# Optimization experiments

Measured on AMD Instinct MI355X. Metric: run time of the kernel, lower is better.

Reference implementation:

```python
import jax, jax.numpy as jnp
import numpy as np
import math

IN_CH = 512
OUT_CH = 512
KSIZE = 3
W_DIM = 512
CONV_SCALE = 1.0 / math.sqrt(IN_CH * KSIZE * KSIZE)
MOD_SCALE = 1.0 / math.sqrt(W_DIM)


def setup_inputs() -> dict:
    key = jax.random.key(0)
    k1, k2, k3, k4 = jax.random.split(key, 4)
    B, H, W = 16, 64, 64
    return {
        "input": jax.random.normal(k1, (B, IN_CH, H, W), dtype=jnp.float32),
        "style": jax.random.normal(k2, (B, W_DIM), dtype=jnp.float32),
        "weight": jax.random.normal(k3, (1, OUT_CH, IN_CH, KSIZE, KSIZE), dtype=jnp.float32),
        "mod_weight": jax.random.normal(k4, (IN_CH, W_DIM), dtype=jnp.float32),
        "mod_bias": jnp.ones((IN_CH,), dtype=jnp.float32),
    }


def reference(input, style, weight, mod_weight, mod_bias):
    B, Cin, H, Wd = input.shape
    # EqualLinear modulation: style -> per-sample, per-input-channel scale
    s = style @ (mod_weight * MOD_SCALE).T + mod_bias  # [B, Cin]
    s = s[:, None, :, None, None]                      # [B,1,Cin,1,1]
    w = CONV_SCALE * weight * s                        # [B,Cout,Cin,k,k]
    demod = jax.lax.rsqrt(jnp.sum(w * w, axis=(2, 3, 4)) + 1e-8)  # [B,Cout]
    w = w * demod[:, :, None, None, None]
    # Grouped conv with groups=batch, same as torch F.conv2d
    w = w.reshape(B * OUT_CH, Cin, KSIZE, KSIZE)
    x = input.reshape(1, B * Cin, H, Wd)
    pad = KSIZE // 2
    out = jax.lax.conv_general_dilated(
        x, w,
        window_strides=(1, 1),
        padding=[(pad, pad), (pad, pad)],
        dimension_numbers=("NCHW", "OIHW", "NCHW"),
        feature_group_count=B,
    )
    return out.reshape(B, OUT_CH, out.shape[2], out.shape[3])
```

## Files before the change

### kernel.cpp

```cpp
#include <hip/hip_runtime.h>
#include <hip/hip_bf16.h>


constexpr float CONV_SCALE = 0.014731391274719738f;
constexpr float MOD_SCALE  = 0.04419417382415922f;

typedef short  bf16x8 __attribute__((ext_vector_type(8)));
typedef float  f32x4  __attribute__((ext_vector_type(4)));

__device__ __forceinline__ unsigned short f2bf(float f) {
  unsigned u = __float_as_uint(f);
  u += 0x7fffu + ((u >> 16) & 1u);
  return (unsigned short)(u >> 16);
}

__device__ __forceinline__ void async16(const void* g, void* l) {
  __builtin_amdgcn_global_load_lds((const __attribute__((address_space(1))) unsigned int*)g,
                                   (__attribute__((address_space(3))) unsigned int*)l,
                                   16, 0, 0);
}

__global__ void k_style(const float* __restrict__ style, const float* __restrict__ mw,
                        const float* __restrict__ mb, float* __restrict__ s) {
  int t = blockIdx.x * 256 + threadIdx.x;
  int b = t & 15, i = t >> 4;
  const float4* st = (const float4*)(style + b * 512);
  const float4* wr = (const float4*)(mw + i * 512);
  float acc = 0.f;
#pragma unroll 8
  for (int j = 0; j < 128; ++j) {
    float4 a = st[j], w4 = wr[j];
    acc += a.x * w4.x + a.y * w4.y + a.z * w4.z + a.w * w4.w;
  }
  s[b * 512 + i] = acc * MOD_SCALE + mb[i];
}

__global__ void k_prepw(const float* __restrict__ w, float* __restrict__ wsq,
                        unsigned short* __restrict__ wt) {
  __shared__ float Wl[2304];
  int t = threadIdx.x;
  size_t base = (size_t)blockIdx.x * 2304;
#pragma unroll
  for (int k = 0; k < 3; ++k) {
    int idx = t + k * 256;
    if (idx < 576) ((float4*)Wl)[idx] = ((const float4*)(w + base))[idx];
  }
  __syncthreads();
  int g = blockIdx.x * 256 + t;
  int ic = g & 511, o = g >> 9;
  float ssq = 0.f;
#pragma unroll
  for (int tap = 0; tap < 9; ++tap) {
    float v = Wl[t * 9 + tap];
    ssq += v * v;
    wt[((size_t)tap * 512 + o) * 512 + ic] = f2bf(v);
  }
  wsq[o * 512 + ic] = ssq;
}

__global__ void k_dscale(const float* __restrict__ s, const float* __restrict__ wsq,
                         float* __restrict__ dscale) {
  int t = blockIdx.x * 256 + threadIdx.x;
  int b = t & 15, o = t >> 4;
  const float4* sq = (const float4*)(wsq + o * 512);
  const float4* sb = (const float4*)(s + b * 512);
  float acc = 0.f;
#pragma unroll 8
  for (int j = 0; j < 128; ++j) {
    float4 q4 = sq[j], s4 = sb[j];
    acc += q4.x * s4.x * s4.x + q4.y * s4.y * s4.y + q4.z * s4.z * s4.z + q4.w * s4.w * s4.w;
  }
  float d = rsqrtf(CONV_SCALE * CONV_SCALE * acc + 1e-8f);
  dscale[b * 512 + o] = d * CONV_SCALE;
}

__global__ void k_zpad(unsigned short* __restrict__ xt) {
  int strip = blockIdx.x;
  int b = strip >> 1, sel = strip & 1;
  unsigned short* p = xt + ((size_t)(b * 66 + sel * 65) * 64) * 512;
  int4 z = {0, 0, 0, 0};
  for (int idx = threadIdx.x; idx < 4096; idx += 256)
    ((int4*)p)[idx] = z;
}

__global__ void k_xt(const float* __restrict__ x, const float* __restrict__ s,
                     unsigned short* __restrict__ xt) {
  int h = blockIdx.x, b = blockIdx.y;
  const float* xp = x + (size_t)b * 512 * 4096 + h * 64;
  unsigned short* xo = xt + ((size_t)(b * 66 + h + 1) * 64) * 512;
  int t = threadIdx.x;
  int o8 = t >> 4, wq = t & 15;
  for (int ic0 = 0; ic0 < 512; ic0 += 128) {
    int icb = ic0 + o8 * 8;
    float4 v[8];
    float sc[8];
#pragma unroll
    for (int r = 0; r < 8; ++r) {
      v[r] = *(const float4*)&xp[(size_t)(icb + r) * 4096 + wq * 4];
      sc[r] = s[b * 512 + icb + r];
    }
#pragma unroll
    for (int j = 0; j < 4; ++j) {
      unsigned pk[4];
#pragma unroll
      for (int p = 0; p < 4; ++p) {
        float lo = ((const float*)&v[2 * p])[j]     * sc[2 * p];
        float hi = ((const float*)&v[2 * p + 1])[j] * sc[2 * p + 1];
        pk[p] = (unsigned)f2bf(lo) | ((unsigned)f2bf(hi) << 16);
      }
      *(uint4*)&xo[(size_t)(wq * 4 + j) * 512 + icb] = *(uint4*)pk;
    }
  }
}

__global__ __launch_bounds__(512, 2)
void k_conv(const unsigned short* __restrict__ xt, const unsigned short* __restrict__ wt,
            const float* __restrict__ dscale, float* __restrict__ out) {
  __shared__ short Xs[2][10 * 66 * 32];
  __shared__ short Wf[9 * 128 * 32];

  const int lin = blockIdx.x;
  const int k8 = lin & 7, jj = lin >> 3;
  const int o0 = (k8 >> 1) * 128;
  const int b  = ((k8 & 1) << 3) | (jj >> 3);
  const int h0 = (jj & 7) * 8;
  const int t = threadIdx.x;
  const int wave = t >> 6, lane = t & 63;
  const int q = lane >> 4, l16 = lane & 15;

  const int xsrc8 = ((lane & 3) ^ ((((lane >> 2) + 1) >> 1) & 3)) * 8;
  const int wsrc8 = ((lane & 3) ^ ((lane >> 3) & 3)) * 8;
  const int wq8 = (q ^ ((l16 >> 1) & 3)) * 8;

  f32x4 acc[8][4];
#pragma unroll
  for (int i = 0; i < 8; ++i)
#pragma unroll
    for (int j = 0; j < 4; ++j) acc[i][j] = (f32x4){0.f, 0.f, 0.f, 0.f};

  for (int z = t; z < 640; z += 512) {
    int bi = (z >= 320) ? 1 : 0;
    int zz = z - bi * 320;
    int r = zz >> 5, rem = zz & 31;
    int col = (rem >> 4) * 65, ch2 = (rem & 15) * 2;
    *(int*)&Xs[bi][(r * 66 + col) * 32 + ch2] = 0;
  }

  auto stageX = [&](int i_, int xb_) {
    int ic0_ = i_ * 32;
#pragma unroll
    for (int j2 = 0; j2 < 5; ++j2) {
      int c = wave * 5 + j2;
      int row = c >> 2, q16 = c & 3;
      async16(xt + ((size_t)((b * 66 + h0 + row) * 64) + q16 * 16 + (lane >> 2)) * 512 + ic0_ + xsrc8,
              &Xs[xb_][(row * 66 + 1 + q16 * 16) * 32]);
    }
  };
  auto stageW = [&](int i_) {
    int ic0_ = i_ * 32;
#pragma unroll
    for (int j2 = 0; j2 < 9; ++j2) {
      int ci = wave * 9 + j2;
      int plane = ci >> 3, oo = ((ci & 7) << 4) + (lane >> 2);
      async16(wt + (((size_t)plane * 512 + o0 + oo) * 512 + ic0_ + wsrc8),
              &Wf[ci * 512]);
    }
  };
  auto compute = [&](int kh, int cur) {
    const short* Xrow = &Xs[cur][(wave + kh) * 66 * 32];
    __builtin_amdgcn_s_setprio(1);
#pragma unroll
    for (int kw = 0; kw < 3; ++kw) {
      bf16x8 bfr[4];
#pragma unroll
      for (int ni = 0; ni < 4; ++ni) {
        int c = ni * 16 + l16 + kw;
        bfr[ni] = *(const bf16x8*)&Xrow[c * 32 + ((q ^ ((c >> 1) & 3)) << 3)];
      }
#pragma unroll
      for (int mi = 0; mi < 8; ++mi) {
        bf16x8 af = *(const bf16x8*)&Wf[((kh * 3 + kw) * 128 + mi * 16 + l16) * 32 + wq8];
#pragma unroll
        for (int ni = 0; ni < 4; ++ni)
          acc[mi][ni] = __builtin_amdgcn_mfma_f32_16x16x32_bf16(af, bfr[ni], acc[mi][ni], 0, 0, 0);
      }
    }
    __builtin_amdgcn_s_setprio(0);
  };

  stageX(0, 0);
  __syncthreads();

  for (int i = 0; i < 16; ++i) {
    const int cur = i & 1;
    stageW(i);
    if (i < 15) {
      stageX(i + 1, cur ^ 1);
      asm volatile("s_waitcnt vmcnt(5)" ::: "memory");
    } else {
      asm volatile("s_waitcnt vmcnt(0)" ::: "memory");
    }
    __builtin_amdgcn_s_barrier();
    compute(0, cur);
    compute(1, cur);
    compute(2, cur);
    __syncthreads();
  }

  const int h = h0 + wave;
#pragma unroll
  for (int mi = 0; mi < 8; ++mi)
#pragma unroll
    for (int r = 0; r < 4; ++r) {
      int o_l = mi * 16 + q * 4 + r;
      float ds = dscale[b * 512 + o0 + o_l];
      float* orow = out + ((size_t)(b * 512 + o0 + o_l) * 64 + h) * 64;
#pragma unroll
      for (int ni = 0; ni < 4; ++ni)
        orow[ni * 16 + l16] = acc[mi][ni][r] * ds;
    }
}

extern "C" void kernel_launch(void* const* d_in, const int* in_sizes, int n_in,
                              void* d_out, int out_size, void* d_ws, size_t ws_size,
                              hipStream_t stream) {
  const float* x      = (const float*)d_in[0];
  const float* style  = (const float*)d_in[1];
  const float* weight = (const float*)d_in[2];
  const float* mw     = (const float*)d_in[3];
  const float* mb     = (const float*)d_in[4];
  float* out = (float*)d_out;

  float* s      = (float*)d_ws;
  float* dscale = s + 8192;
  float* wsq    = dscale + 8192;
  unsigned short* wt = (unsigned short*)(wsq + 262144);
  unsigned short* xt = wt + 9 * 512 * 512;

  k_style<<<32, 256, 0, stream>>>(style, mw, mb, s);
  k_prepw<<<1024, 256, 0, stream>>>(weight, wsq, wt);
  k_dscale<<<32, 256, 0, stream>>>(s, wsq, dscale);
  k_zpad<<<32, 256, 0, stream>>>(xt);
  k_xt<<<dim3(64, 16), 256, 0, stream>>>(x, s, xt);
  k_conv<<<512, 512, 0, stream>>>(xt, wt, dscale, out);
}
```

Baseline: 528.6 us.

## Load conv weights from global in MFMA fragment layout, merge small prep kernels

Weights are pre-packed into an MFMA-fragment-ordered layout so each lane reads its A operand directly from global/L2, removing the LDS weight staging and its barrier waits. The style and demod kernels are merged into one, and the zero-padding is folded into the transpose kernel, cutting launches. The main risk is that the per-kw global loads of weights sit on the critical path without prefetch, which could stall the MFMA pipeline. It also raises global/L2 traffic, since every wave reloads the weight fragments instead of sharing them through LDS.

```diff
diff --git a/kernel.cpp b/kernel.cpp
--- a/kernel.cpp
+++ b/kernel.cpp
@@ -20,75 +20,74 @@
                                    16, 0, 0);
 }
 
-__global__ void k_style(const float* __restrict__ style, const float* __restrict__ mw,
-                        const float* __restrict__ mb, float* __restrict__ s) {
-  int t = blockIdx.x * 256 + threadIdx.x;
-  int b = t & 15, i = t >> 4;
+__global__ void k_prepw(const float* __restrict__ w, float* __restrict__ wsq,
+                        unsigned short* __restrict__ wt2) {
+  __shared__ float Wl[2304];
+  int t = threadIdx.x;
+  size_t base = (size_t)blockIdx.x * 2304;
+#pragma unroll
+  for (int k = 0; k < 3; ++k) {
+    int idx = t + k * 256;
+    if (idx < 576) ((float4*)Wl)[idx] = ((const float4*)(w + base))[idx];
+  }
+  __syncthreads();
+  int g = blockIdx.x * 256 + t;
+  int ic = g & 511, o = g >> 9;
+  int lane8 = ((ic >> 3) & 3) * 16 + (o & 15);
+  float ssq = 0.f;
+#pragma unroll
+  for (int tap = 0; tap < 9; ++tap) {
+    float v = Wl[t * 9 + tap];
+    ssq += v * v;
+    size_t fidx = (size_t)((tap * 16 + (ic >> 5)) * 32 + (o >> 4));
+    wt2[fidx * 512 + lane8 * 8 + (ic & 7)] = f2bf(v);
+  }
+  wsq[o * 512 + ic] = ssq;
+}
+
+__global__ void k_mod(const float* __restrict__ style, const float* __restrict__ mw,
+                      const float* __restrict__ mb, const float* __restrict__ wsq,
+                      float* __restrict__ s_out, float* __restrict__ dscale) {
+  __shared__ float sl[512];
+  int b = blockIdx.x, t = threadIdx.x;
   const float4* st = (const float4*)(style + b * 512);
-  const float4* wr = (const float4*)(mw + i * 512);
+  const float4* wr = (const float4*)(mw + t * 512);
   float acc = 0.f;
 #pragma unroll 8
   for (int j = 0; j < 128; ++j) {
     float4 a = st[j], w4 = wr[j];
     acc += a.x * w4.x + a.y * w4.y + a.z * w4.z + a.w * w4.w;
   }
-  s[b * 512 + i] = acc * MOD_SCALE + mb[i];
-}
-
-__global__ void k_prepw(const float* __restrict__ w, float* __restrict__ wsq,
-                        unsigned short* __restrict__ wt) {
-  __shared__ float Wl[2304];
-  int t = threadIdx.x;
-  size_t base = (size_t)blockIdx.x * 2304;
-#pragma unroll
-  for (int k = 0; k < 3; ++k) {
-    int idx = t + k * 256;
-    if (idx < 576) ((float4*)Wl)[idx] = ((const float4*)(w + base))[idx];
-  }
+  float sv = acc * MOD_SCALE + mb[t];
+  sl[t] = sv;
+  s_out[b * 512 + t] = sv;
   __syncthreads();
-  int g = blockIdx.x * 256 + t;
-  int ic = g & 511, o = g >> 9;
-  float ssq = 0.f;
-#pragma unroll
-  for (int tap = 0; tap < 9; ++tap) {
-    float v = Wl[t * 9 + tap];
-    ssq += v * v;
-    wt[((size_t)tap * 512 + o) * 512 + ic] = f2bf(v);
-  }
-  wsq[o * 512 + ic] = ssq;
-}
-
-__global__ void k_dscale(const float* __restrict__ s, const float* __restrict__ wsq,
-                         float* __restrict__ dscale) {
-  int t = blockIdx.x * 256 + threadIdx.x;
-  int b = t & 15, o = t >> 4;
-  const float4* sq = (const float4*)(wsq + o * 512);
-  const float4* sb = (const float4*)(s + b * 512);
-  float acc = 0.f;
+  const float4* sq = (const float4*)(wsq + t * 512);
+  float a2 = 0.f;
 #pragma unroll 8
   for (int j = 0; j < 128; ++j) {
-    float4 q4 = sq[j], s4 = sb[j];
-    acc += q4.x * s4.x * s4.x + q4.y * s4.y * s4.y + q4.z * s4.z * s4.z + q4.w * s4.w * s4.w;
-  }
-  float d = rsqrtf(CONV_SCALE * CONV_SCALE * acc + 1e-8f);
-  dscale[b * 512 + o] = d * CONV_SCALE;
-}
-
-__global__ void k_zpad(unsigned short* __restrict__ xt) {
-  int strip = blockIdx.x;
-  int b = strip >> 1, sel = strip & 1;
-  unsigned short* p = xt + ((size_t)(b * 66 + sel * 65) * 64) * 512;
-  int4 z = {0, 0, 0, 0};
-  for (int idx = threadIdx.x; idx < 4096; idx += 256)
-    ((int4*)p)[idx] = z;
+    float4 q4 = sq[j];
+    float4 s4 = *(const float4*)&sl[j * 4];
+    a2 += q4.x * s4.x * s4.x + q4.y * s4.y * s4.y + q4.z * s4.z * s4.z + q4.w * s4.w * s4.w;
+  }
+  dscale[b * 512 + t] = rsqrtf(CONV_SCALE * CONV_SCALE * a2 + 1e-8f) * CONV_SCALE;
 }
 
 __global__ void k_xt(const float* __restrict__ x, const float* __restrict__ s,
                      unsigned short* __restrict__ xt) {
   int h = blockIdx.x, b = blockIdx.y;
+  int t = threadIdx.x;
+  if (h == 0) {
+    unsigned short* p = xt + (size_t)(b * 66) * 64 * 512;
+    int4 z = {0, 0, 0, 0};
+    for (int idx = t; idx < 4096; idx += 256) ((int4*)p)[idx] = z;
+  } else if (h == 63) {
+    unsigned short* p = xt + (size_t)(b * 66 + 65) * 64 * 512;
+    int4 z = {0, 0, 0, 0};
+    for (int idx = t; idx < 4096; idx += 256) ((int4*)p)[idx] = z;
+  }
   const float* xp = x + (size_t)b * 512 * 4096 + h * 64;
   unsigned short* xo = xt + ((size_t)(b * 66 + h + 1) * 64) * 512;
-  int t = threadIdx.x;
   int o8 = t >> 4, wq = t & 15;
   for (int ic0 = 0; ic0 < 512; ic0 += 128) {
     int icb = ic0 + o8 * 8;
@@ -114,10 +113,9 @@
 }
 
 __global__ __launch_bounds__(512, 2)
-void k_conv(const unsigned short* __restrict__ xt, const unsigned short* __restrict__ wt,
+void k_conv(const unsigned short* __restrict__ xt, const unsigned short* __restrict__ wt2,
             const float* __restrict__ dscale, float* __restrict__ out) {
   __shared__ short Xs[2][10 * 66 * 32];
-  __shared__ short Wf[9 * 128 * 32];
 
   const int lin = blockIdx.x;
   const int k8 = lin & 7, jj = lin >> 3;
@@ -129,8 +127,7 @@
   const int q = lane >> 4, l16 = lane & 15;
 
   const int xsrc8 = ((lane & 3) ^ ((((lane >> 2) + 1) >> 1) & 3)) * 8;
-  const int wsrc8 = ((lane & 3) ^ ((lane >> 3) & 3)) * 8;
-  const int wq8 = (q ^ ((l16 >> 1) & 3)) * 8;
+  const int fo = o0 >> 4;
 
   f32x4 acc[8][4];
 #pragma unroll
@@ -156,54 +153,37 @@
               &Xs[xb_][(row * 66 + 1 + q16 * 16) * 32]);
     }
   };
-  auto stageW = [&](int i_) {
-    int ic0_ = i_ * 32;
-#pragma unroll
-    for (int j2 = 0; j2 < 9; ++j2) {
-      int ci = wave * 9 + j2;
-      int plane = ci >> 3, oo = ((ci & 7) << 4) + (lane >> 2);
-      async16(wt + (((size_t)plane * 512 + o0 + oo) * 512 + ic0_ + wsrc8),
-              &Wf[ci * 512]);
-    }
-  };
-  auto compute = [&](int kh, int cur) {
-    const short* Xrow = &Xs[cur][(wave + kh) * 66 * 32];
-    __builtin_amdgcn_s_setprio(1);
-#pragma unroll
-    for (int kw = 0; kw < 3; ++kw) {
-      bf16x8 bfr[4];
-#pragma unroll
-      for (int ni = 0; ni < 4; ++ni) {
-        int c = ni * 16 + l16 + kw;
-        bfr[ni] = *(const bf16x8*)&Xrow[c * 32 + ((q ^ ((c >> 1) & 3)) << 3)];
-      }
-#pragma unroll
-      for (int mi = 0; mi < 8; ++mi) {
-        bf16x8 af = *(const bf16x8*)&Wf[((kh * 3 + kw) * 128 + mi * 16 + l16) * 32 + wq8];
-#pragma unroll
-        for (int ni = 0; ni < 4; ++ni)
-          acc[mi][ni] = __builtin_amdgcn_mfma_f32_16x16x32_bf16(af, bfr[ni], acc[mi][ni], 0, 0, 0);
-      }
-    }
-    __builtin_amdgcn_s_setprio(0);
-  };
 
   stageX(0, 0);
   __syncthreads();
 
   for (int i = 0; i < 16; ++i) {
     const int cur = i & 1;
-    stageW(i);
-    if (i < 15) {
-      stageX(i + 1, cur ^ 1);
-      asm volatile("s_waitcnt vmcnt(5)" ::: "memory");
-    } else {
-      asm volatile("s_waitcnt vmcnt(0)" ::: "memory");
-    }
-    __builtin_amdgcn_s_barrier();
-    compute(0, cur);
-    compute(1, cur);
-    compute(2, cur);
+    if (i < 15) stageX(i + 1, cur ^ 1);
+    for (int kh = 0; kh < 3; ++kh) {
+      const short* Xrow = &Xs[cur][(wave + kh) * 66 * 32];
+#pragma unroll
+      for (int kw = 0; kw < 3; ++kw) {
+        const unsigned short* fp =
+            wt2 + ((size_t)(((kh * 3 + kw) * 16 + i) * 32 + fo)) * 512 + lane * 8;
+        bf16x8 af[8];
+#pragma unroll
+        for (int mi = 0; mi < 8; ++mi) af[mi] = *(const bf16x8*)&fp[mi * 512];
+        bf16x8 bfr[4];
+#pragma unroll
+        for (int ni = 0; ni < 4; ++ni) {
+          int c = ni * 16 + l16 + kw;
+          bfr[ni] = *(const bf16x8*)&Xrow[c * 32 + ((q ^ ((c >> 1) & 3)) << 3)];
+        }
+        __builtin_amdgcn_s_setprio(1);
+#pragma unroll
+        for (int mi = 0; mi < 8; ++mi)
+#pragma unroll
+          for (int ni = 0; ni < 4; ++ni)
+            acc[mi][ni] = __builtin_amdgcn_mfma_f32_16x16x32_bf16(af[mi], bfr[ni], acc[mi][ni], 0, 0, 0);
+        __builtin_amdgcn_s_setprio(0);
+      }
+    }
     __syncthreads();
   }
 
@@ -234,13 +214,11 @@
   float* s      = (float*)d_ws;
   float* dscale = s + 8192;
   float* wsq    = dscale + 8192;
-  unsigned short* wt = (unsigned short*)(wsq + 262144);
-  unsigned short* xt = wt + 9 * 512 * 512;
-
-  k_style<<<32, 256, 0, stream>>>(style, mw, mb, s);
-  k_prepw<<<1024, 256, 0, stream>>>(weight, wsq, wt);
-  k_dscale<<<32, 256, 0, stream>>>(s, wsq, dscale);
-  k_zpad<<<32, 256, 0, stream>>>(xt);
+  unsigned short* wt2 = (unsigned short*)(wsq + 262144);
+  unsigned short* xt = wt2 + 9 * 512 * 512;
+
+  k_prepw<<<1024, 256, 0, stream>>>(weight, wsq, wt2);
+  k_mod<<<16, 512, 0, stream>>>(style, mw, mb, wsq, s, dscale);
   k_xt<<<dim3(64, 16), 256, 0, stream>>>(x, s, xt);
-  k_conv<<<512, 512, 0, stream>>>(xt, wt, dscale, out);
-}
+  k_conv<<<512, 512, 0, stream>>>(xt, wt2, dscale, out);
+}
```

Result: no change. 537.9 us (+1.7%).
